# Performance work log

Measured on AMD Instinct MI355X. Metric: run time of the kernel, lower is better.

Reference implementation:

```python
import jax, jax.numpy as jnp
import numpy as np

N_NODES = 100000
N_EDGES = 1600000
N_GRAPHS = 1024
HID = 32
EPS = 1e-5


def gcn_conv(x, W, b, row, col):
    # PyG GCNConv: h = x @ W, then symmetric-normalized scatter-add over
    # edges (self-loops already included in row/col).
    h = x @ W  # [N, out]
    deg = jax.ops.segment_sum(jnp.ones_like(col, dtype=h.dtype), col, num_segments=N_NODES)
    dinv = jnp.where(deg > 0, jax.lax.rsqrt(jnp.maximum(deg, 1.0)), 0.0)
    norm = dinv[row] * dinv[col]  # [E+N]
    msg = h[row] * norm[:, None]
    out = jax.ops.segment_sum(msg, col, num_segments=N_NODES)
    return out + b


def graph_norm(x, batch, weight, bias, mean_scale):
    # PyG GraphNorm: per-graph mean/var with learnable mean scale.
    ones = jnp.ones((x.shape[0], 1), dtype=x.dtype)
    cnt = jnp.maximum(jax.ops.segment_sum(ones, batch, num_segments=N_GRAPHS), 1.0)  # [G,1]
    mean = jax.ops.segment_sum(x, batch, num_segments=N_GRAPHS) / cnt
    out = x - mean[batch] * mean_scale
    var = jax.ops.segment_sum(out * out, batch, num_segments=N_GRAPHS) / cnt
    std = jnp.sqrt(var + EPS)
    return weight * out / std[batch] + bias


def setup_inputs() -> dict:
    key = jax.random.key(0)
    ks = jax.random.split(key, 16)
    x = jax.random.normal(ks[0], (N_NODES, 3), dtype=jnp.float32)
    edge_index = jax.random.randint(ks[1], (2, N_EDGES), 0, N_NODES, dtype=jnp.int64)
    batch = jnp.sort(jax.random.randint(ks[2], (N_NODES,), 0, N_GRAPHS, dtype=jnp.int64))
    def lin_init(k, fan_in, shape):
        bound = 1.0 / np.sqrt(fan_in)
        return jax.random.uniform(k, shape, jnp.float32, -bound, bound)
    params = {
        "W1": lin_init(ks[3], 3, (3, HID)), "b1": lin_init(ks[4], 3, (HID,)),
        "W2": lin_init(ks[5], HID, (HID, HID)), "b2": lin_init(ks[6], HID, (HID,)),
        "W3": lin_init(ks[7], HID, (HID, HID)), "b3": lin_init(ks[8], HID, (HID,)),
        "g1": jnp.ones((HID,)), "be1": jnp.zeros((HID,)), "ms1": jnp.ones((HID,)),
        "g2": jnp.ones((HID,)), "be2": jnp.zeros((HID,)), "ms2": jnp.ones((HID,)),
        "g3": jnp.ones((HID,)), "be3": jnp.zeros((HID,)), "ms3": jnp.ones((HID,)),
        "Wl": lin_init(ks[9], HID, (HID, 3)), "bl": lin_init(ks[10], HID, (3,)),
    }
    return {"x": x, "edge_index": edge_index, "batch": batch, **params}


def reference(x, edge_index, batch, W1, b1, W2, b2, W3, b3,
              g1, be1, ms1, g2, be2, ms2, g3, be3, ms3, Wl, bl):
    # Eval mode: dropouts / feature mask / edge dropout are identity.
    loops = jnp.arange(N_NODES, dtype=edge_index.dtype)
    row = jnp.concatenate([edge_index[0], loops])
    col = jnp.concatenate([edge_index[1], loops])

    x1 = jax.nn.relu(graph_norm(gcn_conv(x, W1, b1, row, col), batch, g1, be1, ms1))
    h2 = graph_norm(gcn_conv(x1, W2, b2, row, col), batch, g2, be2, ms2)
    x2 = jax.nn.relu(h2 + x1)
    h3 = graph_norm(gcn_conv(x2, W3, b3, row, col), batch, g3, be3, ms3)
    x3 = jax.nn.relu(h3 + x2)

    pooled = jax.ops.segment_sum(x3, batch, num_segments=N_GRAPHS)  # [G, HID]
    counts = jax.ops.segment_sum(jnp.ones((N_NODES,), jnp.float32), batch, num_segments=N_GRAPHS)
    pooled = pooled / jnp.maximum(counts, 1.0)[:, None]
    return pooled @ Wl + bl  # [G, 3]
```

## Files before the change

### kernel.cpp

```cpp
#include <hip/hip_runtime.h>
#include <hip/hip_fp16.h>


#define NN 100000
#define NE 1600000
#define NG 1024
#define HD 32
#define EPSV 1e-5f

__global__ __launch_bounds__(256) void k_bound(const int* __restrict__ batch,
                                               int* __restrict__ gstart) {
    int v = blockIdx.x * 256 + threadIdx.x;
    if (v >= NN) return;
    int b = batch[v];
    int bp = (v > 0) ? batch[v - 1] : -1;
    for (int g = bp + 1; g <= b; g++) gstart[g] = v;
    if (v == NN - 1)
        for (int g = b + 1; g <= NG; g++) gstart[g] = NN;
}

__global__ __launch_bounds__(256) void k_count(const int* __restrict__ col,
                                               int* __restrict__ deg) {
    int e = blockIdx.x * 256 + threadIdx.x;
    if (e < NE) atomicAdd(&deg[col[e]], 1);
}

__global__ __launch_bounds__(256) void k_alloc(const int* __restrict__ deg,
                                               int* __restrict__ start,
                                               float* __restrict__ dinv,
                                               int* __restrict__ counter) {
    int v = blockIdx.x * 256 + threadIdx.x;
    int lane = threadIdx.x & 63;
    int d = (v < NN) ? (deg[v] + 1) : 0;
    int incl = d;
    #pragma unroll
    for (int off = 1; off < 64; off <<= 1) {
        int n = __shfl_up(incl, off);
        if (lane >= off) incl += n;
    }
    int total = __shfl(incl, 63);
    int base = 0;
    if (lane == 63) base = atomicAdd(counter, total);
    base = __shfl(base, 63);
    if (v < NN) {
        start[v] = base + incl - d;
        dinv[v] = rsqrtf((float)d);
    }
}

__global__ __launch_bounds__(256) void k_fill(const int* __restrict__ row,
                                              const int* __restrict__ col,
                                              const int* __restrict__ start,
                                              int* __restrict__ fill,
                                              int* __restrict__ csr_src) {
    int e = blockIdx.x * 256 + threadIdx.x;
    if (e >= NE + NN) return;
    int r, c;
    if (e < NE) { r = row[e]; c = col[e]; }
    else        { r = e - NE; c = r; }
    int pos = start[c] + atomicAdd(&fill[c], 1);
    csr_src[pos] = r;
}

template <int K>
__global__ __launch_bounds__(256) void k_premul(const float* __restrict__ xin,
                                                const float* __restrict__ W,
                                                const float* __restrict__ dinv,
                                                __half* __restrict__ hs) {
    __shared__ float sW[K * HD];
    for (int i = threadIdx.x; i < K * HD; i += 256) sW[i] = W[i];
    __syncthreads();
    int t = blockIdx.x * 256 + threadIdx.x;
    int v = t >> 2, o = t & 3;
    if (v >= NN) return;
    const float* xv = xin + (size_t)v * K;
    float acc[8] = {0.f, 0.f, 0.f, 0.f, 0.f, 0.f, 0.f, 0.f};
    #pragma unroll
    for (int k = 0; k < K; k++) {
        float xk = xv[k];
        #pragma unroll
        for (int j = 0; j < 8; j++) acc[j] += xk * sW[k * HD + o * 8 + j];
    }
    float dv = dinv[v];
    __half2 h[4];
    #pragma unroll
    for (int j = 0; j < 4; j++)
        h[j] = __floats2half2_rn(dv * acc[2 * j], dv * acc[2 * j + 1]);
    *reinterpret_cast<float4*>(hs + (size_t)v * HD + o * 8) = *reinterpret_cast<float4*>(h);
}

__global__ __launch_bounds__(256) void k_gather(const __half* __restrict__ hs,
                                                const int* __restrict__ csr_src,
                                                const int* __restrict__ start,
                                                const int* __restrict__ deg,
                                                const float* __restrict__ dinv,
                                                const float* __restrict__ bias,
                                                float* __restrict__ outb) {
    int wid = (blockIdx.x * 256 + threadIdx.x) >> 6;
    if (wid >= NN) return;
    int lane = threadIdx.x & 63;
    int q = lane & 3;
    int es = lane >> 2;
    int s = start[wid], d = deg[wid] + 1;
    float acc[8] = {0.f, 0.f, 0.f, 0.f, 0.f, 0.f, 0.f, 0.f};
    for (int i = es; i < d; i += 16) {
        int src = csr_src[s + i];
        float4 raw = *reinterpret_cast<const float4*>(hs + (size_t)src * HD + q * 8);
        const __half2* hp = reinterpret_cast<const __half2*>(&raw);
        #pragma unroll
        for (int j = 0; j < 4; j++) {
            float2 f2 = __half22float2(hp[j]);
            acc[2 * j]     += f2.x;
            acc[2 * j + 1] += f2.y;
        }
    }
    #pragma unroll
    for (int off = 4; off < 64; off <<= 1) {
        #pragma unroll
        for (int j = 0; j < 8; j++) acc[j] += __shfl_xor(acc[j], off);
    }
    if (es == 0) {
        float dv = dinv[wid];
        float4 w0, w1;
        w0.x = bias[q * 8 + 0] + dv * acc[0];
        w0.y = bias[q * 8 + 1] + dv * acc[1];
        w0.z = bias[q * 8 + 2] + dv * acc[2];
        w0.w = bias[q * 8 + 3] + dv * acc[3];
        w1.x = bias[q * 8 + 4] + dv * acc[4];
        w1.y = bias[q * 8 + 5] + dv * acc[5];
        w1.z = bias[q * 8 + 6] + dv * acc[6];
        w1.w = bias[q * 8 + 7] + dv * acc[7];
        float* op = outb + (size_t)wid * HD + q * 8;
        *reinterpret_cast<float4*>(op)     = w0;
        *reinterpret_cast<float4*>(op + 4) = w1;
    }
}

template <bool RES, bool POOL>
__global__ __launch_bounds__(256) void k_gnorm(const float* __restrict__ o,
                                               const int* __restrict__ gstart,
                                               const float* __restrict__ gamma,
                                               const float* __restrict__ beta,
                                               const float* __restrict__ msc,
                                               const float* __restrict__ xprev,
                                               float* __restrict__ xout,
                                               const float* __restrict__ Wl,
                                               const float* __restrict__ bl,
                                               float* __restrict__ outf) {
    int g = blockIdx.x;
    int s = gstart[g], e = gstart[g + 1];
    int f = threadIdx.x & 31, nl = threadIdx.x >> 5;
    float as = 0.f, aq = 0.f;
    for (int v = s + nl; v < e; v += 8) {
        float xv = o[(size_t)v * HD + f];
        as += xv;
        aq += xv * xv;
    }
    __shared__ float ls[256], lq[256];
    __shared__ float sA[HD], sB[HD];
    ls[threadIdx.x] = as;
    lq[threadIdx.x] = aq;
    __syncthreads();
    if (threadIdx.x < HD) {
        float ss = 0.f, qq = 0.f;
        #pragma unroll
        for (int k = 0; k < 8; k++) { ss += ls[k * 32 + f]; qq += lq[k * 32 + f]; }
        float inv = 1.f / fmaxf((float)(e - s), 1.f);
        float m = ss * inv, mq = qq * inv, ms = msc[f];
        float var = mq - m * m * ms * (2.f - ms);
        float A = gamma[f] * rsqrtf(var + EPSV);
        sA[f] = A;
        sB[f] = beta[f] - A * m * ms;
    }
    __syncthreads();
    float A = sA[f], B = sB[f];
    float pool = 0.f;
    for (int v = s + nl; v < e; v += 8) {
        float xv = o[(size_t)v * HD + f];
        float y = A * xv + B;
        if (RES) y += xprev[(size_t)v * HD + f];
        y = fmaxf(y, 0.f);
        xout[(size_t)v * HD + f] = y;
        if (POOL) pool += y;
    }
    if (POOL) {
        __syncthreads();
        ls[threadIdx.x] = pool;
        __syncthreads();
        if (threadIdx.x < HD) {
            float ss = 0.f;
            #pragma unroll
            for (int k = 0; k < 8; k++) ss += ls[k * 32 + f];
            lq[f] = ss / fmaxf((float)(e - s), 1.f);
        }
        __syncthreads();
        if (threadIdx.x < 3) {
            float acc = bl[threadIdx.x];
            #pragma unroll
            for (int f2 = 0; f2 < HD; f2++) acc += lq[f2] * Wl[f2 * 3 + threadIdx.x];
            outf[g * 3 + threadIdx.x] = acc;
        }
    }
}

extern "C" void kernel_launch(void* const* d_in, const int* in_sizes, int n_in,
                              void* d_out, int out_size, void* d_ws, size_t ws_size,
                              hipStream_t stream) {
    const float* x     = (const float*)d_in[0];
    const int*   ei    = (const int*)d_in[1];
    const int*   batch = (const int*)d_in[2];
    const float* W1 = (const float*)d_in[3];
    const float* b1 = (const float*)d_in[4];
    const float* W2 = (const float*)d_in[5];
    const float* b2 = (const float*)d_in[6];
    const float* W3 = (const float*)d_in[7];
    const float* b3 = (const float*)d_in[8];
    const float* g1 = (const float*)d_in[9];
    const float* be1 = (const float*)d_in[10];
    const float* ms1 = (const float*)d_in[11];
    const float* g2 = (const float*)d_in[12];
    const float* be2 = (const float*)d_in[13];
    const float* ms2 = (const float*)d_in[14];
    const float* g3 = (const float*)d_in[15];
    const float* be3 = (const float*)d_in[16];
    const float* ms3 = (const float*)d_in[17];
    const float* Wl = (const float*)d_in[18];
    const float* bl = (const float*)d_in[19];
    float* out = (float*)d_out;

    const int* row = ei;
    const int* col = ei + NE;

    char* ws = (char*)d_ws;
    size_t off = 0;
    int*   fill    = (int*)(ws + off);   off += (size_t)NN * 4;
    int*   deg     = (int*)(ws + off);   off += (size_t)NN * 4;
    int*   counter = (int*)(ws + off);   off += 16;
    size_t zero_bytes = off;
    int*   start   = (int*)(ws + off);   off += (size_t)NN * 4;
    float* dinv    = (float*)(ws + off); off += (size_t)NN * 4;
    int*   gstart  = (int*)(ws + off);   off += (size_t)(NG + 4) * 4;
    int*   csr_src = (int*)(ws + off);   off += (size_t)(NE + NN) * 4;
    __half* bufH   = (__half*)(ws + off); off += (size_t)NN * HD * 2;
    float* bufO    = (float*)(ws + off); off += (size_t)NN * HD * 4;
    float* bufX    = (float*)(ws + off); off += (size_t)NN * HD * 4;
    (void)ws_size; (void)in_sizes; (void)n_in; (void)out_size;

    hipMemsetAsync(ws, 0, zero_bytes, stream);

    const int nb_n   = (NN + 255) / 256;
    const int nb_e   = (NE + 255) / 256;
    const int nb_et  = (NE + NN + 255) / 256;
    const int nb_no  = (NN * 4 + 255) / 256;
    const int nb_gw  = (NN * 64 + 255) / 256;

    k_bound<<<nb_n, 256, 0, stream>>>(batch, gstart);
    k_count<<<nb_e, 256, 0, stream>>>(col, deg);
    k_alloc<<<nb_n, 256, 0, stream>>>(deg, start, dinv, counter);
    k_fill <<<nb_et, 256, 0, stream>>>(row, col, start, fill, csr_src);

    k_premul<3><<<nb_no, 256, 0, stream>>>(x, W1, dinv, bufH);
    k_gather<<<nb_gw, 256, 0, stream>>>(bufH, csr_src, start, deg, dinv, b1, bufO);
    k_gnorm<false, false><<<NG, 256, 0, stream>>>(bufO, gstart, g1, be1, ms1,
                                                  nullptr, bufX, nullptr, nullptr, nullptr);

    k_premul<HD><<<nb_no, 256, 0, stream>>>(bufX, W2, dinv, bufH);
    k_gather<<<nb_gw, 256, 0, stream>>>(bufH, csr_src, start, deg, dinv, b2, bufO);
    k_gnorm<true, false><<<NG, 256, 0, stream>>>(bufO, gstart, g2, be2, ms2,
                                                 bufX, bufX, nullptr, nullptr, nullptr);

    k_premul<HD><<<nb_no, 256, 0, stream>>>(bufX, W3, dinv, bufH);
    k_gather<<<nb_gw, 256, 0, stream>>>(bufH, csr_src, start, deg, dinv, b3, bufO);
    k_gnorm<true, true><<<NG, 256, 0, stream>>>(bufO, gstart, g3, be3, ms3,
                                                bufX, bufX, Wl, bl, out);
}
```

Measured before the change: 476.1 us.

## Partition CSR fill into destination-range passes and prefetch first gather edges

The CSR fill kernel now uses a fixed grid of blocks, each owning a contiguous edge chunk, and makes several passes that each scatter only edges whose destination falls in one quarter of the node range. The aim is to keep atomic and scatter targets within a smaller, cache-resident window. The cost is reading row and col several times. The gather kernel also issues its first two neighbour loads unconditionally with masks, so more memory requests are in flight before the loop. Inactive lanes load node 0 and multiply by zero.

```diff
diff --git a/kernel.cpp b/kernel.cpp
--- a/kernel.cpp
+++ b/kernel.cpp
@@ -7,6 +7,10 @@
 #define NG 1024
 #define HD 32
 #define EPSV 1e-5f
+
+#define FILL_PASSES 4
+#define FILL_BLOCKS 2048
+#define NPP ((NN + FILL_PASSES - 1) / FILL_PASSES)
 
 __global__ __launch_bounds__(256) void k_bound(const int* __restrict__ batch,
                                                int* __restrict__ gstart) {
@@ -53,13 +57,23 @@
                                               const int* __restrict__ start,
                                               int* __restrict__ fill,
                                               int* __restrict__ csr_src) {
-    int e = blockIdx.x * 256 + threadIdx.x;
-    if (e >= NE + NN) return;
-    int r, c;
-    if (e < NE) { r = row[e]; c = col[e]; }
-    else        { r = e - NE; c = r; }
-    int pos = start[c] + atomicAdd(&fill[c], 1);
-    csr_src[pos] = r;
+    const int total = NE + NN;
+    const int chunk = (total + FILL_BLOCKS - 1) / FILL_BLOCKS;
+    int c0 = blockIdx.x * chunk;
+    int c1 = min(c0 + chunk, total);
+    for (int pass = 0; pass < FILL_PASSES; pass++) {
+        int lo = pass * NPP;
+        int hi = lo + NPP;
+        for (int e = c0 + threadIdx.x; e < c1; e += 256) {
+            int r, c;
+            if (e < NE) { r = row[e]; c = col[e]; }
+            else        { r = e - NE; c = r; }
+            if (c >= lo && c < hi) {
+                int pos = start[c] + atomicAdd(&fill[c], 1);
+                csr_src[pos] = r;
+            }
+        }
+    }
 }
 
 template <int K>
@@ -103,7 +117,34 @@
     int es = lane >> 2;
     int s = start[wid], d = deg[wid] + 1;
     float acc[8] = {0.f, 0.f, 0.f, 0.f, 0.f, 0.f, 0.f, 0.f};
-    for (int i = es; i < d; i += 16) {
+
+    bool a0 = (es < d);
+    bool a1 = (es + 16 < d);
+    int src0 = a0 ? csr_src[s + es] : 0;
+    int src1 = a1 ? csr_src[s + es + 16] : 0;
+    float4 raw0 = *reinterpret_cast<const float4*>(hs + (size_t)src0 * HD + q * 8);
+    float4 raw1 = *reinterpret_cast<const float4*>(hs + (size_t)src1 * HD + q * 8);
+    float m0 = a0 ? 1.f : 0.f;
+    float m1 = a1 ? 1.f : 0.f;
+    {
+        const __half2* hp = reinterpret_cast<const __half2*>(&raw0);
+        #pragma unroll
+        for (int j = 0; j < 4; j++) {
+            float2 f2 = __half22float2(hp[j]);
+            acc[2 * j]     += m0 * f2.x;
+            acc[2 * j + 1] += m0 * f2.y;
+        }
+    }
+    {
+        const __half2* hp = reinterpret_cast<const __half2*>(&raw1);
+        #pragma unroll
+        for (int j = 0; j < 4; j++) {
+            float2 f2 = __half22float2(hp[j]);
+            acc[2 * j]     += m1 * f2.x;
+            acc[2 * j + 1] += m1 * f2.y;
+        }
+    }
+    for (int i = es + 32; i < d; i += 16) {
         int src = csr_src[s + i];
         float4 raw = *reinterpret_cast<const float4*>(hs + (size_t)src * HD + q * 8);
         const __half2* hp = reinterpret_cast<const __half2*>(&raw);
@@ -250,14 +291,13 @@
 
     const int nb_n   = (NN + 255) / 256;
     const int nb_e   = (NE + 255) / 256;
-    const int nb_et  = (NE + NN + 255) / 256;
     const int nb_no  = (NN * 4 + 255) / 256;
     const int nb_gw  = (NN * 64 + 255) / 256;
 
     k_bound<<<nb_n, 256, 0, stream>>>(batch, gstart);
     k_count<<<nb_e, 256, 0, stream>>>(col, deg);
     k_alloc<<<nb_n, 256, 0, stream>>>(deg, start, dinv, counter);
-    k_fill <<<nb_et, 256, 0, stream>>>(row, col, start, fill, csr_src);
+    k_fill <<<FILL_BLOCKS, 256, 0, stream>>>(row, col, start, fill, csr_src);
 
     k_premul<3><<<nb_no, 256, 0, stream>>>(x, W1, dinv, bufH);
     k_gather<<<nb_gw, 256, 0, stream>>>(bufH, csr_src, start, deg, dinv, b1, bufO);
```

Result: faster. 431.1 us (-9.4%).
